# Performance work log

Hardware: AMD Instinct MI355X
Metric: run time of the kernel (lower is better)

The kernel has to match this reference:

```python
import jax, jax.numpy as jnp
import numpy as np
from math import log2, floor

B, N, DIM = 2, 2048, 2048
HEADS, DIM_HEAD, FF_MULT = 16, 128, 4
RMS_EPS = 1e-8


def _get_slopes(heads):
    def pow2_slopes(n):
        start = 2 ** (-2 ** (-(log2(n) - 3)))
        return [start * start ** i for i in range(n)]
    if log2(heads).is_integer():
        return pow2_slopes(heads)
    closest = 2 ** floor(log2(heads))
    return pow2_slopes(closest) + pow2_slopes(2 * closest)[0::2][: heads - closest]


def setup_inputs() -> dict:
    key = jax.random.key(0)
    ks = jax.random.split(key, 5)
    std = 0.02
    return {
        "x": jax.random.normal(ks[0], (B, N, DIM), dtype=jnp.float32),
        "g": jnp.ones((DIM,), dtype=jnp.float32),
        "w_qkv": jax.random.normal(ks[1], (DIM, DIM + DIM_HEAD), dtype=jnp.float32) * std,
        "w_attn_out": jax.random.normal(ks[2], (DIM, DIM), dtype=jnp.float32) * std,
        "w_ff1": jax.random.normal(ks[3], (DIM, 2 * FF_MULT * DIM), dtype=jnp.float32) * std,
        "w_ff2": jax.random.normal(ks[4], (FF_MULT * DIM, DIM), dtype=jnp.float32) * std,
    }


def reference(x, g, w_qkv, w_attn_out, w_ff1, w_ff2):
    b, n, dim = x.shape
    # RMSNorm: x / clamp(||x|| * dim^-0.5, eps) * g
    norm = jnp.linalg.norm(x, axis=-1, keepdims=True) * (dim ** -0.5)
    xn = x / jnp.maximum(norm, RMS_EPS) * g

    # Parallel SwiGLU FFN branch (shares normed input with attention)
    h = xn @ w_ff1                       # [b, n, 2*ff_mult*dim]
    val, gate = jnp.split(h, 2, axis=-1)
    ff_out = (jax.nn.silu(gate) * val) @ w_ff2  # [b, n, dim]

    # Multi-query attention: single dim_head-wide kv shared as K and V
    qkv = xn @ w_qkv                     # [b, n, dim + dim_head]
    q, kv = qkv[..., :dim], qkv[..., dim:]
    q = q.reshape(b, n, HEADS, DIM_HEAD) * (DIM_HEAD ** -0.5)
    sim = jnp.einsum('bihd,bjd->bhij', q, kv)  # [b, h, n, n]

    # ALiBi bias: -|j - i| * slope_h
    slopes = jnp.asarray(_get_slopes(HEADS), dtype=sim.dtype)[:, None, None]
    pos = jnp.arange(n)
    bias = -jnp.abs(pos[None, None, :] - pos[None, :, None]).astype(sim.dtype) * slopes
    sim = sim + bias

    # Causal mask (strict upper triangle masked)
    causal = jnp.triu(jnp.ones((n, n), dtype=bool), 1)
    neg = jnp.asarray(jnp.finfo(sim.dtype).max, sim.dtype)
    sim = jnp.where(causal, -neg, sim)

    attn = jax.nn.softmax(sim, axis=-1)
    out = jnp.einsum('bhij,bjd->bhid', attn, kv)     # [b, h, n, dim_head]
    out = out.transpose(0, 2, 1, 3).reshape(b, n, dim)
    return out @ w_attn_out + ff_out
```

## Files before the change

kernel.cpp:

```cpp
#include <hip/hip_runtime.h>
#include <stdint.h>

typedef unsigned short u16;
typedef __attribute__((ext_vector_type(8))) short bf16x8;
typedef __attribute__((ext_vector_type(4))) float f32x4;
typedef __attribute__((ext_vector_type(8))) unsigned short us8;
typedef __attribute__((ext_vector_type(4))) float fvec4;

#define BATCH 2
#define SEQ   2048
#define DIMM  2048
#define NH    16
#define DH    128
#define ROWS  (BATCH*SEQ)
#define QKVN  (DIMM + DH)
#define FFH   8192
#define LOG2E 1.44269504088896340736f

static __device__ __forceinline__ u16 f2bf(float x) {
  union { float f; uint32_t u; } v; v.f = x;
  uint32_t r = (v.u + 0x7fffu + ((v.u >> 16) & 1u)) >> 16;
  return (u16)r;
}

static __device__ __forceinline__ float fast_exp2(float x) {
  float r; asm("v_exp_f32 %0, %1" : "=v"(r) : "v"(x)); return r;
}

static __device__ __forceinline__ void gld_lds16(const void* g, void* l) {
  __builtin_amdgcn_global_load_lds(
      (const __attribute__((address_space(1))) uint32_t*)g,
      (__attribute__((address_space(3))) uint32_t*)l, 16, 0, 0);
}

__global__ __launch_bounds__(256)
void rmsnorm_k(const float* __restrict__ x, const float* __restrict__ g, u16* __restrict__ xn) {
  const int row = blockIdx.x;
  const float* xr = x + (size_t)row * DIMM;
  const int off = threadIdx.x * 8;
  fvec4 a = *(const fvec4*)(xr + off);
  fvec4 b = *(const fvec4*)(xr + off + 4);
  float ss = a[0]*a[0]+a[1]*a[1]+a[2]*a[2]+a[3]*a[3]
           + b[0]*b[0]+b[1]*b[1]+b[2]*b[2]+b[3]*b[3];
  #pragma unroll
  for (int m = 32; m >= 1; m >>= 1) ss += __shfl_xor(ss, m);
  __shared__ float red[4];
  if ((threadIdx.x & 63) == 0) red[threadIdx.x >> 6] = ss;
  __syncthreads();
  float tot = red[0] + red[1] + red[2] + red[3];
  float inv = 1.0f / fmaxf(sqrtf(tot * (1.0f / DIMM)), 1e-8f);
  fvec4 ga = *(const fvec4*)(g + off);
  fvec4 gb = *(const fvec4*)(g + off + 4);
  us8 o;
  #pragma unroll
  for (int i = 0; i < 4; i++) { o[i] = f2bf(a[i]*inv*ga[i]); o[4+i] = f2bf(b[i]*inv*gb[i]); }
  *(us8*)(xn + (size_t)row * DIMM + off) = o;
}

template<typename TIN>
__global__ __launch_bounds__(256)
void transpose_to_bf16(const TIN* __restrict__ in, u16* __restrict__ out, int R, int C) {
  __shared__ u16 tile[64 * 65];
  const int r0 = blockIdx.y * 64, c0 = blockIdx.x * 64;
  const int tr = threadIdx.x >> 2;
  const int tc = (threadIdx.x & 3) * 16;
  const TIN* ip = in + (size_t)(r0 + tr) * C + c0 + tc;
  u16 tmp[16];
  #pragma unroll
  for (int i = 0; i < 16; i++) {
    if constexpr (sizeof(TIN) == 4) tmp[i] = f2bf(((const float*)ip)[i]);
    else                            tmp[i] = ((const u16*)ip)[i];
  }
  #pragma unroll
  for (int i = 0; i < 16; i++) tile[tr * 65 + tc + i] = tmp[i];
  __syncthreads();
  const int oc  = c0 + tr;
  const int orr = (threadIdx.x & 3) * 16;
  us8 v0, v1;
  #pragma unroll
  for (int i = 0; i < 8; i++) v0[i] = tile[(orr + i) * 65 + tr];
  #pragma unroll
  for (int i = 0; i < 8; i++) v1[i] = tile[(orr + 8 + i) * 65 + tr];
  u16* op = out + (size_t)oc * R + r0 + orr;
  *(us8*)op = v0;
  *(us8*)(op + 8) = v1;
}

template<int MODE>
__global__ __launch_bounds__(256, 2)
void gemm_bf16(const u16* __restrict__ A, const u16* __restrict__ BT, int K,
               float* __restrict__ outF, u16* __restrict__ outQ, u16* __restrict__ outKV) {
  __shared__ __align__(16) u16 lA[128 * 32];
  __shared__ __align__(16) u16 lB[128 * 32];
  const int tid = threadIdx.x;
  const int wave = tid >> 6, lane = tid & 63;
  const int lid = lane & 15, quad = lane >> 4;
  const int wm = wave >> 1, wn = wave & 1;
  const int row0 = blockIdx.y * 128;
  const int col0 = blockIdx.x * 128;
  f32x4 acc[4][4];
  #pragma unroll
  for (int i = 0; i < 4; i++)
    #pragma unroll
    for (int j = 0; j < 4; j++) { acc[i][j][0]=0.f; acc[i][j][1]=0.f; acc[i][j][2]=0.f; acc[i][j][3]=0.f; }

  const int rA0 = wave * 32;
  const int rsub = lane >> 2;
  const int cl = lane & 3;

  for (int k0 = 0; k0 < K; k0 += 32) {
    #pragma unroll
    for (int h2 = 0; h2 < 2; ++h2) {
      int rloc = rA0 + h2 * 16 + rsub;
      int gc = cl ^ ((rloc >> 1) & 3);
      gld_lds16(A  + (size_t)(row0 + rloc) * K + k0 + gc * 8, lA + (rA0 + h2 * 16) * 32);
      gld_lds16(BT + (size_t)(col0 + rloc) * K + k0 + gc * 8, lB + (rA0 + h2 * 16) * 32);
    }
    __syncthreads();
    bf16x8 af[4], bfr[4];
    #pragma unroll
    for (int i = 0; i < 4; i++) {
      int r  = wm * 64 + i * 16 + lid;
      af[i]  = *(const bf16x8*)(lA + r * 32 + (quad ^ ((r >> 1) & 3)) * 8);
      int rb = wn * 64 + i * 16 + lid;
      bfr[i] = *(const bf16x8*)(lB + rb * 32 + (quad ^ ((rb >> 1) & 3)) * 8);
    }
    #pragma unroll
    for (int im = 0; im < 4; im++)
      #pragma unroll
      for (int in = 0; in < 4; in++)
        acc[im][in] = __builtin_amdgcn_mfma_f32_16x16x32_bf16(af[im], bfr[in], acc[im][in], 0, 0, 0);
    __syncthreads();
  }

  #pragma unroll
  for (int im = 0; im < 4; im++)
    #pragma unroll
    for (int in = 0; in < 4; in++) {
      int col = col0 + wn * 64 + in * 16 + lid;
      int rbase = row0 + wm * 64 + im * 16 + quad * 4;
      #pragma unroll
      for (int rg = 0; rg < 4; rg++) {
        float v = acc[im][in][rg];
        int row = rbase + rg;
        if constexpr (MODE == 0) {
          if (col < DIMM) outQ[(size_t)row * DIMM + col] = f2bf(v);
          else            outKV[(size_t)row * DH + (col - DIMM)] = f2bf(v);
        } else if constexpr (MODE == 2) {
          outF[(size_t)row * DIMM + col] = v;
        } else {
          outF[(size_t)row * DIMM + col] += v;
        }
      }
    }
}

__global__ __launch_bounds__(256, 2)
void gemm_ff1_swiglu(const u16* __restrict__ A, const u16* __restrict__ BT, u16* __restrict__ FF) {
  __shared__ __align__(16) u16 lA[128 * 32];
  __shared__ __align__(16) u16 lB[128 * 32];
  const int tid = threadIdx.x;
  const int wave = tid >> 6, lane = tid & 63;
  const int lid = lane & 15, quad = lane >> 4;
  const int wm = wave >> 1, wn = wave & 1;
  const int row0 = blockIdx.y * 128;
  const int n0 = blockIdx.x * 64;
  const int K = DIMM;
  f32x4 av[4][2], ag[4][2];
  #pragma unroll
  for (int i = 0; i < 4; i++)
    #pragma unroll
    for (int j = 0; j < 2; j++) {
      av[i][j][0]=0.f; av[i][j][1]=0.f; av[i][j][2]=0.f; av[i][j][3]=0.f;
      ag[i][j][0]=0.f; ag[i][j][1]=0.f; ag[i][j][2]=0.f; ag[i][j][3]=0.f;
    }
  const int rA0 = wave * 32;
  const int rsub = lane >> 2, cl = lane & 3;

  for (int k0 = 0; k0 < K; k0 += 32) {
    #pragma unroll
    for (int h2 = 0; h2 < 2; ++h2) {
      int rloc = rA0 + h2 * 16 + rsub;
      int gc = cl ^ ((rloc >> 1) & 3);
      int grow = (rloc < 64) ? (n0 + rloc) : (FFH + n0 + rloc - 64);
      gld_lds16(A  + (size_t)(row0 + rloc) * K + k0 + gc * 8, lA + (rA0 + h2 * 16) * 32);
      gld_lds16(BT + (size_t)grow * K + k0 + gc * 8,          lB + (rA0 + h2 * 16) * 32);
    }
    __syncthreads();
    bf16x8 af[4], bv[2], bg[2];
    #pragma unroll
    for (int i = 0; i < 4; i++) {
      int r = wm * 64 + i * 16 + lid;
      af[i] = *(const bf16x8*)(lA + r * 32 + (quad ^ ((r >> 1) & 3)) * 8);
    }
    #pragma unroll
    for (int i = 0; i < 2; i++) {
      int rv = wn * 32 + i * 16 + lid;
      bv[i] = *(const bf16x8*)(lB + rv * 32 + (quad ^ ((rv >> 1) & 3)) * 8);
      int rg2 = 64 + wn * 32 + i * 16 + lid;
      bg[i] = *(const bf16x8*)(lB + rg2 * 32 + (quad ^ ((rg2 >> 1) & 3)) * 8);
    }
    #pragma unroll
    for (int im = 0; im < 4; im++)
      #pragma unroll
      for (int in = 0; in < 2; in++) {
        av[im][in] = __builtin_amdgcn_mfma_f32_16x16x32_bf16(af[im], bv[in], av[im][in], 0, 0, 0);
        ag[im][in] = __builtin_amdgcn_mfma_f32_16x16x32_bf16(af[im], bg[in], ag[im][in], 0, 0, 0);
      }
    __syncthreads();
  }

  #pragma unroll
  for (int im = 0; im < 4; im++)
    #pragma unroll
    for (int in = 0; in < 2; in++) {
      int col = n0 + wn * 32 + in * 16 + lid;
      int rbase = row0 + wm * 64 + im * 16 + quad * 4;
      #pragma unroll
      for (int rg = 0; rg < 4; rg++) {
        float vv = av[im][in][rg];
        float gg = ag[im][in][rg];
        float sig = 1.0f / (1.0f + fast_exp2(-gg * LOG2E));
        FF[(size_t)(rbase + rg) * FFH + col] = f2bf(vv * gg * sig);
      }
    }
}

__global__ __launch_bounds__(256, 1)
void attn_k2(const u16* __restrict__ qws, const u16* __restrict__ kvws,
             const u16* __restrict__ kvt, u16* __restrict__ attnws) {
  __shared__ __align__(16) u16 kvls[128 * 128];
  __shared__ __align__(16) u16 kvtls[128 * 128];
  __shared__ __align__(16) u16 plds[4][32][136];
  const int tid = threadIdx.x;
  const int wave = tid >> 6, lane = tid & 63;
  const int lid = lane & 15, quad = lane >> 4;
  const int hb = blockIdx.y;
  const int h = hb & (NH - 1), b = hb >> 4;
  const int pair = blockIdx.x;
  const float slope2 = fast_exp2(-0.5f * (float)(h + 1)) * LOG2E;
  const float scale2 = 0.08838834764831845f * LOG2E;
  const float NEG = -__builtin_inff();

  const u16* kvb  = kvws + (size_t)b * SEQ * DH;
  const u16* kvtb = kvt  + (size_t)b * DH * SEQ;

  #pragma unroll 1
  for (int tt = 0; tt < 2; tt++) {
    const int T = tt ? (15 - pair) : pair;
    const int rw = T * 128 + wave * 32;

    bf16x8 qf[2][4];
    #pragma unroll
    for (int ig = 0; ig < 2; ig++)
      #pragma unroll
      for (int ks = 0; ks < 4; ks++)
        qf[ig][ks] = *(const bf16x8*)(qws + (size_t)(b * SEQ + rw + ig * 16 + lid) * DIMM
                                       + h * DH + ks * 32 + quad * 8);
    float srow2[2][4];
    #pragma unroll
    for (int ig = 0; ig < 2; ig++)
      #pragma unroll
      for (int rg = 0; rg < 4; rg++)
        srow2[ig][rg] = slope2 * (float)(rw + ig * 16 + quad * 4 + rg);

    f32x4 o[2][8];
    #pragma unroll
    for (int ig = 0; ig < 2; ig++)
      #pragma unroll
      for (int nd = 0; nd < 8; nd++) { o[ig][nd][0]=0.f; o[ig][nd][1]=0.f; o[ig][nd][2]=0.f; o[ig][nd][3]=0.f; }
    float m2[2][4], l[2][4];
    #pragma unroll
    for (int ig = 0; ig < 2; ig++)
      #pragma unroll
      for (int rg = 0; rg < 4; rg++) { m2[ig][rg] = NEG; l[ig][rg] = 0.f; }

    const int njt = T + 1;
    #pragma unroll 1
    for (int jt = 0; jt < njt; jt++) {
      const int j0 = jt * 128;
      __syncthreads();
      {
        const int c = lane & 15;
        const int r4 = lane >> 4;
        #pragma unroll
        for (int it = 0; it < 8; it++) {
          const int r = wave * 32 + it * 4 + r4;
          const int gc = c ^ (r & 15);
          gld_lds16(kvb  + (size_t)(j0 + r) * DH + gc * 8,        kvls  + (wave * 32 + it * 4) * 128);
          gld_lds16(kvtb + (size_t)r * SEQ + j0 + gc * 8,         kvtls + (wave * 32 + it * 4) * 128);
        }
      }
      __syncthreads();

      const int rhi = rw + 31;
      const int nbmax = min(8, ((rhi - j0) >> 4) + 1);
      const int ks2max = (nbmax + 1) >> 1;

      float pvv[2][8][4];
      float mt[2][4];
      #pragma unroll
      for (int ig = 0; ig < 2; ig++)
        #pragma unroll
        for (int rg = 0; rg < 4; rg++) mt[ig][rg] = NEG;

      #pragma unroll
      for (int nb = 0; nb < 8; nb++) {
        if (nb < nbmax) {
          bf16x8 bk[4];
          #pragma unroll
          for (int ks = 0; ks < 4; ks++)
            bk[ks] = *(const bf16x8*)(kvls + (nb * 16 + lid) * 128 + (((ks * 4 + quad) ^ lid) << 3));
          f32x4 s0, s1;
          s0[0]=0.f;s0[1]=0.f;s0[2]=0.f;s0[3]=0.f;
          s1[0]=0.f;s1[1]=0.f;s1[2]=0.f;s1[3]=0.f;
          #pragma unroll
          for (int ks = 0; ks < 4; ks++) {
            s0 = __builtin_amdgcn_mfma_f32_16x16x32_bf16(qf[0][ks], bk[ks], s0, 0, 0, 0);
            s1 = __builtin_amdgcn_mfma_f32_16x16x32_bf16(qf[1][ks], bk[ks], s1, 0, 0, 0);
          }
          const int jl = j0 + nb * 16 + lid;
          const float sj = slope2 * (float)jl;
          #pragma unroll
          for (int rg = 0; rg < 4; rg++) {
            const int row0r = rw + quad * 4 + rg;
            float e0 = fmaf(s0[rg], scale2, sj) - srow2[0][rg];
            e0 = (jl <= row0r) ? e0 : NEG;
            pvv[0][nb][rg] = e0;
            mt[0][rg] = fmaxf(mt[0][rg], e0);
            float e1 = fmaf(s1[rg], scale2, sj) - srow2[1][rg];
            e1 = (jl <= row0r + 16) ? e1 : NEG;
            pvv[1][nb][rg] = e1;
            mt[1][rg] = fmaxf(mt[1][rg], e1);
          }
        }
      }

      float alpha[2][4];
      #pragma unroll
      for (int ig = 0; ig < 2; ig++)
        #pragma unroll
        for (int rg = 0; rg < 4; rg++) {
          float m = mt[ig][rg];
          m = fmaxf(m, __shfl_xor(m, 1));
          m = fmaxf(m, __shfl_xor(m, 2));
          m = fmaxf(m, __shfl_xor(m, 4));
          m = fmaxf(m, __shfl_xor(m, 8));
          float mn = fmaxf(m2[ig][rg], m);
          alpha[ig][rg] = fast_exp2(m2[ig][rg] - mn);
          m2[ig][rg] = mn;
        }

      float rs[2][4];
      #pragma unroll
      for (int ig = 0; ig < 2; ig++)
        #pragma unroll
        for (int rg = 0; rg < 4; rg++) rs[ig][rg] = 0.f;
      #pragma unroll
      for (int nb = 0; nb < 8; nb++) {
        if (nb < nbmax) {
          #pragma unroll
          for (int ig = 0; ig < 2; ig++)
            #pragma unroll
            for (int rg = 0; rg < 4; rg++) {
              float p = fast_exp2(pvv[ig][nb][rg] - m2[ig][rg]);
              rs[ig][rg] += p;
              plds[wave][ig * 16 + quad * 4 + rg][nb * 16 + lid] = f2bf(p);
            }
        }
      }
      if (nbmax & 1) {
        #pragma unroll
        for (int ig = 0; ig < 2; ig++)
          #pragma unroll
          for (int rg = 0; rg < 4; rg++)
            plds[wave][ig * 16 + quad * 4 + rg][nbmax * 16 + lid] = 0;
      }

      #pragma unroll
      for (int ig = 0; ig < 2; ig++)
        #pragma unroll
        for (int rg = 0; rg < 4; rg++) {
          float r = rs[ig][rg];
          r += __shfl_xor(r, 1);
          r += __shfl_xor(r, 2);
          r += __shfl_xor(r, 4);
          r += __shfl_xor(r, 8);
          l[ig][rg] = l[ig][rg] * alpha[ig][rg] + r;
        }
      #pragma unroll
      for (int ig = 0; ig < 2; ig++)
        #pragma unroll
        for (int nd = 0; nd < 8; nd++)
          #pragma unroll
          for (int rg = 0; rg < 4; rg++) o[ig][nd][rg] *= alpha[ig][rg];

      asm volatile("s_waitcnt lgkmcnt(0)" ::: "memory");
      #pragma unroll
      for (int ks2 = 0; ks2 < 4; ks2++) {
        if (ks2 < ks2max) {
          bf16x8 pa0 = *(const bf16x8*)&plds[wave][lid][ks2 * 32 + quad * 8];
          bf16x8 pa1 = *(const bf16x8*)&plds[wave][16 + lid][ks2 * 32 + quad * 8];
          #pragma unroll
          for (int nd = 0; nd < 8; nd++) {
            bf16x8 bv = *(const bf16x8*)(kvtls + (nd * 16 + lid) * 128 + (((ks2 * 4 + quad) ^ lid) << 3));
            o[0][nd] = __builtin_amdgcn_mfma_f32_16x16x32_bf16(pa0, bv, o[0][nd], 0, 0, 0);
            o[1][nd] = __builtin_amdgcn_mfma_f32_16x16x32_bf16(pa1, bv, o[1][nd], 0, 0, 0);
          }
        }
      }
    }

    #pragma unroll
    for (int ig = 0; ig < 2; ig++) {
      float inv[4];
      #pragma unroll
      for (int rg = 0; rg < 4; rg++) inv[rg] = 1.0f / l[ig][rg];
      #pragma unroll
      for (int nd = 0; nd < 8; nd++)
        #pragma unroll
        for (int rg = 0; rg < 4; rg++) {
          int row = rw + ig * 16 + quad * 4 + rg;
          attnws[(size_t)(b * SEQ + row) * DIMM + h * DH + nd * 16 + lid] =
              f2bf(o[ig][nd][rg] * inv[rg]);
        }
    }
  }
}

extern "C" void kernel_launch(void* const* d_in, const int* in_sizes, int n_in,
                              void* d_out, int out_size, void* d_ws, size_t ws_size,
                              hipStream_t stream) {
  (void)in_sizes; (void)n_in; (void)out_size; (void)ws_size;
  const float* x     = (const float*)d_in[0];
  const float* g     = (const float*)d_in[1];
  const float* w_qkv = (const float*)d_in[2];
  const float* w_ao  = (const float*)d_in[3];
  const float* w_ff1 = (const float*)d_in[4];
  const float* w_ff2 = (const float*)d_in[5];
  float* out = (float*)d_out;

  u16* ws = (u16*)d_ws;
  u16* xn     = ws;
  u16* wTqkv  = xn     + 8388608;
  u16* wTattn = wTqkv  + 4456448;
  u16* wTff1  = wTattn + 4194304;
  u16* wTff2  = wTff1  + 33554432;
  u16* ffin   = wTff2  + 16777216;
  u16* qws    = ffin   + 33554432;
  u16* kvws   = qws    + 8388608;
  u16* kvtws  = kvws   + 524288;
  u16* attnws = kvtws  + 524288;

  transpose_to_bf16<float><<<dim3(QKVN/64, DIMM/64), 256, 0, stream>>>(w_qkv, wTqkv, DIMM, QKVN);
  transpose_to_bf16<float><<<dim3(DIMM/64, DIMM/64), 256, 0, stream>>>(w_ao, wTattn, DIMM, DIMM);
  transpose_to_bf16<float><<<dim3((2*FFH)/64, DIMM/64), 256, 0, stream>>>(w_ff1, wTff1, DIMM, 2*FFH);
  transpose_to_bf16<float><<<dim3(DIMM/64, FFH/64), 256, 0, stream>>>(w_ff2, wTff2, FFH, DIMM);

  rmsnorm_k<<<ROWS, 256, 0, stream>>>(x, g, xn);

  gemm_bf16<0><<<dim3(QKVN/128, ROWS/128), 256, 0, stream>>>(xn, wTqkv, DIMM, nullptr, qws, kvws);

  transpose_to_bf16<u16><<<dim3(DH/64, SEQ/64), 256, 0, stream>>>(kvws, kvtws, SEQ, DH);
  transpose_to_bf16<u16><<<dim3(DH/64, SEQ/64), 256, 0, stream>>>(kvws + (size_t)SEQ*DH, kvtws + (size_t)DH*SEQ, SEQ, DH);

  attn_k2<<<dim3(8, NH*BATCH), 256, 0, stream>>>(qws, kvws, kvtws, attnws);

  gemm_ff1_swiglu<<<dim3(FFH/64, ROWS/128), 256, 0, stream>>>(xn, wTff1, ffin);
  gemm_bf16<2><<<dim3(DIMM/128, ROWS/128), 256, 0, stream>>>(ffin, wTff2, FFH, out, nullptr, nullptr);

  gemm_bf16<3><<<dim3(DIMM/128, ROWS/128), 256, 0, stream>>>(attnws, wTattn, DIMM, out, nullptr, nullptr);
}
```

Before: 1.034 ms.

## Fuse QKV with FF1-SwiGLU GEMM and FF2 with attention-out GEMM

Merges the QKV projection and the SwiGLU FF1 GEMM into one launch whose grid splits blocks between the two jobs, since both read the same normed input. It also concatenates the FF2 and attention-output GEMMs along K into a single kernel that writes the output once, removing the float read-modify-write of the output. This cuts launches, fills the GPU better for the small QKV GEMM, and saves output traffic. The cost is per-iteration branching and a unified accumulator layout in the fused kernels.

```diff
diff --git a/kernel.cpp b/kernel.cpp
--- a/kernel.cpp
+++ b/kernel.cpp
@@ -86,10 +86,103 @@
   *(us8*)(op + 8) = v1;
 }
 
-template<int MODE>
 __global__ __launch_bounds__(256, 2)
-void gemm_bf16(const u16* __restrict__ A, const u16* __restrict__ BT, int K,
-               float* __restrict__ outF, u16* __restrict__ outQ, u16* __restrict__ outKV) {
+void gemm1_fused(const u16* __restrict__ A, const u16* __restrict__ BTff1,
+                 const u16* __restrict__ BTqkv, u16* __restrict__ FF,
+                 u16* __restrict__ outQ, u16* __restrict__ outKV) {
+  __shared__ __align__(16) u16 lA[128 * 32];
+  __shared__ __align__(16) u16 lB[128 * 32];
+  const int tid = threadIdx.x;
+  const int wave = tid >> 6, lane = tid & 63;
+  const int lid = lane & 15, quad = lane >> 4;
+  const int wm = wave >> 1, wn = wave & 1;
+  const int row0 = blockIdx.y * 128;
+  const bool isff = (blockIdx.x < 128);
+  const int n0   = blockIdx.x * 64;
+  const int col0 = (blockIdx.x - 128) * 128;
+  const int K = DIMM;
+
+  f32x4 acc[4][4];
+  #pragma unroll
+  for (int i = 0; i < 4; i++)
+    #pragma unroll
+    for (int j = 0; j < 4; j++) { acc[i][j][0]=0.f; acc[i][j][1]=0.f; acc[i][j][2]=0.f; acc[i][j][3]=0.f; }
+
+  const int rA0 = wave * 32;
+  const int rsub = lane >> 2;
+  const int cl = lane & 3;
+
+  int rbrow[4];
+  #pragma unroll
+  for (int in = 0; in < 4; in++)
+    rbrow[in] = isff ? ((in < 2) ? (wn * 32 + in * 16) : (64 + wn * 32 + (in - 2) * 16))
+                     : (wn * 64 + in * 16);
+
+  for (int k0 = 0; k0 < K; k0 += 32) {
+    #pragma unroll
+    for (int h2 = 0; h2 < 2; ++h2) {
+      int rloc = rA0 + h2 * 16 + rsub;
+      int gc = cl ^ ((rloc >> 1) & 3);
+      int grow = isff ? ((rloc < 64) ? (n0 + rloc) : (FFH + n0 + rloc - 64))
+                      : (col0 + rloc);
+      gld_lds16(A + (size_t)(row0 + rloc) * K + k0 + gc * 8, lA + (rA0 + h2 * 16) * 32);
+      gld_lds16((isff ? BTff1 : BTqkv) + (size_t)grow * K + k0 + gc * 8,
+                lB + (rA0 + h2 * 16) * 32);
+    }
+    __syncthreads();
+    bf16x8 af[4], bfr[4];
+    #pragma unroll
+    for (int i = 0; i < 4; i++) {
+      int r  = wm * 64 + i * 16 + lid;
+      af[i]  = *(const bf16x8*)(lA + r * 32 + (quad ^ ((r >> 1) & 3)) * 8);
+      int rb = rbrow[i] + lid;
+      bfr[i] = *(const bf16x8*)(lB + rb * 32 + (quad ^ ((rb >> 1) & 3)) * 8);
+    }
+    #pragma unroll
+    for (int im = 0; im < 4; im++)
+      #pragma unroll
+      for (int in = 0; in < 4; in++)
+        acc[im][in] = __builtin_amdgcn_mfma_f32_16x16x32_bf16(af[im], bfr[in], acc[im][in], 0, 0, 0);
+    __syncthreads();
+  }
+
+  if (isff) {
+    #pragma unroll
+    for (int im = 0; im < 4; im++)
+      #pragma unroll
+      for (int in = 0; in < 2; in++) {
+        int col = n0 + wn * 32 + in * 16 + lid;
+        int rbase = row0 + wm * 64 + im * 16 + quad * 4;
+        #pragma unroll
+        for (int rg = 0; rg < 4; rg++) {
+          float vv = acc[im][in][rg];
+          float gg = acc[im][in + 2][rg];
+          float sig = 1.0f / (1.0f + fast_exp2(-gg * LOG2E));
+          FF[(size_t)(rbase + rg) * FFH + col] = f2bf(vv * gg * sig);
+        }
+      }
+  } else {
+    #pragma unroll
+    for (int im = 0; im < 4; im++)
+      #pragma unroll
+      for (int in = 0; in < 4; in++) {
+        int col = col0 + wn * 64 + in * 16 + lid;
+        int rbase = row0 + wm * 64 + im * 16 + quad * 4;
+        #pragma unroll
+        for (int rg = 0; rg < 4; rg++) {
+          float v = acc[im][in][rg];
+          int row = rbase + rg;
+          if (col < DIMM) outQ[(size_t)row * DIMM + col] = f2bf(v);
+          else            outKV[(size_t)row * DH + (col - DIMM)] = f2bf(v);
+        }
+      }
+  }
+}
+
+__global__ __launch_bounds__(256, 2)
+void gemm2_fused(const u16* __restrict__ Aff, const u16* __restrict__ Aat,
+                 const u16* __restrict__ BTff2, const u16* __restrict__ BTat,
+                 float* __restrict__ out) {
   __shared__ __align__(16) u16 lA[128 * 32];
   __shared__ __align__(16) u16 lB[128 * 32];
   const int tid = threadIdx.x;
@@ -108,13 +201,18 @@
   const int rsub = lane >> 2;
   const int cl = lane & 3;
 
-  for (int k0 = 0; k0 < K; k0 += 32) {
+  for (int k0 = 0; k0 < FFH + DIMM; k0 += 32) {
+    const bool p1 = (k0 < FFH);
+    const u16* Ab = p1 ? Aff : Aat;
+    const u16* Bb = p1 ? BTff2 : BTat;
+    const int kk = p1 ? k0 : (k0 - FFH);
+    const int ld = p1 ? FFH : DIMM;
     #pragma unroll
     for (int h2 = 0; h2 < 2; ++h2) {
       int rloc = rA0 + h2 * 16 + rsub;
       int gc = cl ^ ((rloc >> 1) & 3);
-      gld_lds16(A  + (size_t)(row0 + rloc) * K + k0 + gc * 8, lA + (rA0 + h2 * 16) * 32);
-      gld_lds16(BT + (size_t)(col0 + rloc) * K + k0 + gc * 8, lB + (rA0 + h2 * 16) * 32);
+      gld_lds16(Ab + (size_t)(row0 + rloc) * ld + kk + gc * 8, lA + (rA0 + h2 * 16) * 32);
+      gld_lds16(Bb + (size_t)(col0 + rloc) * ld + kk + gc * 8, lB + (rA0 + h2 * 16) * 32);
     }
     __syncthreads();
     bf16x8 af[4], bfr[4];
@@ -140,89 +238,8 @@
       int col = col0 + wn * 64 + in * 16 + lid;
       int rbase = row0 + wm * 64 + im * 16 + quad * 4;
       #pragma unroll
-      for (int rg = 0; rg < 4; rg++) {
-        float v = acc[im][in][rg];
-        int row = rbase + rg;
-        if constexpr (MODE == 0) {
-          if (col < DIMM) outQ[(size_t)row * DIMM + col] = f2bf(v);
-          else            outKV[(size_t)row * DH + (col - DIMM)] = f2bf(v);
-        } else if constexpr (MODE == 2) {
-          outF[(size_t)row * DIMM + col] = v;
-        } else {
-          outF[(size_t)row * DIMM + col] += v;
-        }
-      }
-    }
-}
-
-__global__ __launch_bounds__(256, 2)
-void gemm_ff1_swiglu(const u16* __restrict__ A, const u16* __restrict__ BT, u16* __restrict__ FF) {
-  __shared__ __align__(16) u16 lA[128 * 32];
-  __shared__ __align__(16) u16 lB[128 * 32];
-  const int tid = threadIdx.x;
-  const int wave = tid >> 6, lane = tid & 63;
-  const int lid = lane & 15, quad = lane >> 4;
-  const int wm = wave >> 1, wn = wave & 1;
-  const int row0 = blockIdx.y * 128;
-  const int n0 = blockIdx.x * 64;
-  const int K = DIMM;
-  f32x4 av[4][2], ag[4][2];
-  #pragma unroll
-  for (int i = 0; i < 4; i++)
-    #pragma unroll
-    for (int j = 0; j < 2; j++) {
-      av[i][j][0]=0.f; av[i][j][1]=0.f; av[i][j][2]=0.f; av[i][j][3]=0.f;
-      ag[i][j][0]=0.f; ag[i][j][1]=0.f; ag[i][j][2]=0.f; ag[i][j][3]=0.f;
-    }
-  const int rA0 = wave * 32;
-  const int rsub = lane >> 2, cl = lane & 3;
-
-  for (int k0 = 0; k0 < K; k0 += 32) {
-    #pragma unroll
-    for (int h2 = 0; h2 < 2; ++h2) {
-      int rloc = rA0 + h2 * 16 + rsub;
-      int gc = cl ^ ((rloc >> 1) & 3);
-      int grow = (rloc < 64) ? (n0 + rloc) : (FFH + n0 + rloc - 64);
-      gld_lds16(A  + (size_t)(row0 + rloc) * K + k0 + gc * 8, lA + (rA0 + h2 * 16) * 32);
-      gld_lds16(BT + (size_t)grow * K + k0 + gc * 8,          lB + (rA0 + h2 * 16) * 32);
-    }
-    __syncthreads();
-    bf16x8 af[4], bv[2], bg[2];
-    #pragma unroll
-    for (int i = 0; i < 4; i++) {
-      int r = wm * 64 + i * 16 + lid;
-      af[i] = *(const bf16x8*)(lA + r * 32 + (quad ^ ((r >> 1) & 3)) * 8);
-    }
-    #pragma unroll
-    for (int i = 0; i < 2; i++) {
-      int rv = wn * 32 + i * 16 + lid;
-      bv[i] = *(const bf16x8*)(lB + rv * 32 + (quad ^ ((rv >> 1) & 3)) * 8);
-      int rg2 = 64 + wn * 32 + i * 16 + lid;
-      bg[i] = *(const bf16x8*)(lB + rg2 * 32 + (quad ^ ((rg2 >> 1) & 3)) * 8);
-    }
-    #pragma unroll
-    for (int im = 0; im < 4; im++)
-      #pragma unroll
-      for (int in = 0; in < 2; in++) {
-        av[im][in] = __builtin_amdgcn_mfma_f32_16x16x32_bf16(af[im], bv[in], av[im][in], 0, 0, 0);
-        ag[im][in] = __builtin_amdgcn_mfma_f32_16x16x32_bf16(af[im], bg[in], ag[im][in], 0, 0, 0);
-      }
-    __syncthreads();
-  }
-
-  #pragma unroll
-  for (int im = 0; im < 4; im++)
-    #pragma unroll
-    for (int in = 0; in < 2; in++) {
-      int col = n0 + wn * 32 + in * 16 + lid;
-      int rbase = row0 + wm * 64 + im * 16 + quad * 4;
-      #pragma unroll
-      for (int rg = 0; rg < 4; rg++) {
-        float vv = av[im][in][rg];
-        float gg = ag[im][in][rg];
-        float sig = 1.0f / (1.0f + fast_exp2(-gg * LOG2E));
-        FF[(size_t)(rbase + rg) * FFH + col] = f2bf(vv * gg * sig);
-      }
+      for (int rg = 0; rg < 4; rg++)
+        out[(size_t)(rbase + rg) * DIMM + col] = acc[im][in][rg];
     }
 }
 
@@ -459,15 +476,14 @@
 
   rmsnorm_k<<<ROWS, 256, 0, stream>>>(x, g, xn);
 
-  gemm_bf16<0><<<dim3(QKVN/128, ROWS/128), 256, 0, stream>>>(xn, wTqkv, DIMM, nullptr, qws, kvws);
+  gemm1_fused<<<dim3(FFH/64 + QKVN/128, ROWS/128), 256, 0, stream>>>(
+      xn, wTff1, wTqkv, ffin, qws, kvws);
 
   transpose_to_bf16<u16><<<dim3(DH/64, SEQ/64), 256, 0, stream>>>(kvws, kvtws, SEQ, DH);
   transpose_to_bf16<u16><<<dim3(DH/64, SEQ/64), 256, 0, stream>>>(kvws + (size_t)SEQ*DH, kvtws + (size_t)DH*SEQ, SEQ, DH);
 
   attn_k2<<<dim3(8, NH*BATCH), 256, 0, stream>>>(qws, kvws, kvtws, attnws);
 
-  gemm_ff1_swiglu<<<dim3(FFH/64, ROWS/128), 256, 0, stream>>>(xn, wTff1, ffin);
-  gemm_bf16<2><<<dim3(DIMM/128, ROWS/128), 256, 0, stream>>>(ffin, wTff2, FFH, out, nullptr, nullptr);
-
-  gemm_bf16<3><<<dim3(DIMM/128, ROWS/128), 256, 0, stream>>>(attnws, wTattn, DIMM, out, nullptr, nullptr);
-}
+  gemm2_fused<<<dim3(DIMM/128, ROWS/128), 256, 0, stream>>>(
+      ffin, attnws, wTff2, wTattn, out);
+}
```

Result: slower. 1.086 ms (+5.0%).
